# Kernel tuning notes

Measured on AMD Instinct MI355X. Metric: run time of the kernel, lower is better.

## Reference

```python
import jax, jax.numpy as jnp
import numpy as np

IN_DIM = 1024
HID = 256
OUT_DIM = 1000
NUM_BINS = 51
BATCH = 2048
N_LEGAL = 200


def setup_inputs() -> dict:
    key = jax.random.key(0)
    ks = jax.random.split(key, 12)
    s = lambda fan_in: 1.0 / np.sqrt(fan_in)
    u = lambda k, shp, b: jax.random.uniform(k, shp, jnp.float32, -b, b)
    return {
        "x": jax.random.normal(ks[0], (BATCH, IN_DIM), jnp.float32),
        # weights stored as [in, out] (math-equivalent to torch Linear)
        "w_in": u(ks[1], (IN_DIM, HID), s(IN_DIM)),
        "b_in": u(ks[2], (HID,), s(IN_DIM)),
        "w_ah": u(ks[3], (HID, HID), s(HID)),
        "b_ah": u(ks[4], (HID,), s(HID)),
        "w_ao": u(ks[5], (HID, OUT_DIM * NUM_BINS), s(HID)),
        "b_ao": u(ks[6], (OUT_DIM * NUM_BINS,), s(HID)),
        "w_vh": u(ks[7], (HID, HID), s(HID)),
        "b_vh": u(ks[8], (HID,), s(HID)),
        "w_vo": u(ks[9], (HID, NUM_BINS), s(HID)),
        "b_vo": u(ks[10], (NUM_BINS,), s(HID)),
        "v_range": jnp.linspace(-10.0, 10.0, NUM_BINS, dtype=jnp.float32),
        "possible_moves": jax.random.randint(ks[11], (BATCH, N_LEGAL), 0, OUT_DIM),
    }


def reference(x, w_in, b_in, w_ah, b_ah, w_ao, b_ao, w_vh, b_vh, w_vo, b_vo,
              v_range, possible_moves):
    B = x.shape[0]
    h = jax.nn.relu(x @ w_in + b_in)                       # [B, 256]
    adv_h = jax.nn.relu(h @ w_ah + b_ah)                   # [B, 256]
    val_h = jax.nn.relu(h @ w_vh + b_vh)                   # [B, 256]
    adv = (adv_h @ w_ao + b_ao).reshape(B, OUT_DIM, NUM_BINS)
    val = (val_h @ w_vo + b_vo).reshape(B, 1, NUM_BINS)
    q = val + adv - adv.mean(axis=1, keepdims=True)        # [B, A, bins]
    p = jnp.maximum(jax.nn.softmax(q, axis=2), 1e-5)       # softmax + clamp(min=1e-5)
    q_vals = jnp.sum(p * v_range, axis=2)                  # [B, A]
    # LegalSoftmax: per-row scatter of 1.0 at legal indices, vectorized
    mask = jnp.zeros((B, OUT_DIM), x.dtype).at[
        jnp.arange(B)[:, None], possible_moves].set(1.0)
    filtered = q_vals * mask
    # faithful to torch: any exact-zero entry (masked OR coincidental) -> -inf
    return jnp.where(filtered == 0, -jnp.inf, filtered)
```

## Files before the change

kernel.cpp:

```cpp
#include <hip/hip_runtime.h>
#include <cstdint>
#include <cstddef>

#define NB      2048
#define INDIM   1024
#define HID     256
#define NA      1000
#define BINS    51
#define NLEG    200
#define NPAIR   (NB*NLEG)
#define NBLK    256
#define PPB     (NPAIR/NBLK)

#define NEG_SENTINEL (-1.0e30f)

typedef float    f32x4  __attribute__((ext_vector_type(4)));
typedef __bf16   bf16x8 __attribute__((ext_vector_type(8)));
typedef unsigned short us8 __attribute__((ext_vector_type(8)));
typedef unsigned short us4 __attribute__((ext_vector_type(4)));
typedef unsigned long long u64x2 __attribute__((ext_vector_type(2)));

__device__ __forceinline__ unsigned short f2bf(float f) {
  union { float f; unsigned u; } v; v.f = f;
  return (unsigned short)((v.u + 0x7FFFu + ((v.u >> 16) & 1u)) >> 16);
}
__device__ __forceinline__ bf16x8 as_bf(us8 v) { return __builtin_bit_cast(bf16x8, v); }
__device__ __forceinline__ int imin(int a, int b) { return a < b ? a : b; }

__device__ __forceinline__ unsigned f2fp8x4(float a, float b, float c, float d) {
  int v = 0;
  v = __builtin_amdgcn_cvt_pk_fp8_f32(a, b, v, false);
  v = __builtin_amdgcn_cvt_pk_fp8_f32(c, d, v, true);
  return (unsigned)v;
}
__device__ __forceinline__ unsigned char f2fp8(float f) {
  int v = __builtin_amdgcn_cvt_pk_fp8_f32(f, 0.f, 0, false);
  return (unsigned char)(v & 0xff);
}
__device__ __forceinline__ float fp82f(unsigned char u) {
  return __builtin_amdgcn_cvt_f32_fp8((int)u, 0);
}

__global__ __launch_bounds__(256) void k_pre(
    const float* __restrict__ w_ao, unsigned char* __restrict__ wp8,
    float* __restrict__ wmean_acc,
    const float* __restrict__ w_in, const float* __restrict__ w_ah,
    const float* __restrict__ w_vh,
    unsigned short* __restrict__ w_inT, unsigned short* __restrict__ w_ahT,
    unsigned short* __restrict__ w_vhT,
    float* __restrict__ out, const int* __restrict__ pm,
    int* __restrict__ cnt,
    const float* __restrict__ x, unsigned short* __restrict__ x_bf) {
  __shared__ __align__(16) unsigned char smem[16320];
  int b = blockIdx.x, tid = threadIdx.x;
  if (b < 1000) {
    unsigned char* st = smem;
    int s = b & 7, a0 = (b >> 3) * 8;
    const float* wbase = w_ao + (size_t)(s * 32) * (NA * BINS) + a0 * BINS;
    for (int i = tid; i < 816; i += 256) {
      int kq = i / 102, c4 = i - kq * 102;
      const float* rp = wbase + (size_t)(kq * 4) * (NA * BINS) + c4 * 4;
      float4 f0 = *(const float4*)(rp);
      float4 f1 = *(const float4*)(rp + NA * BINS);
      float4 f2 = *(const float4*)(rp + 2 * NA * BINS);
      float4 f3 = *(const float4*)(rp + 3 * NA * BINS);
      unsigned pk0 = f2fp8x4(f0.x * 16.f, f0.y * 16.f, f0.z * 16.f, f0.w * 16.f);
      unsigned pk1 = f2fp8x4(f1.x * 16.f, f1.y * 16.f, f1.z * 16.f, f1.w * 16.f);
      unsigned pk2 = f2fp8x4(f2.x * 16.f, f2.y * 16.f, f2.z * 16.f, f2.w * 16.f);
      unsigned pk3 = f2fp8x4(f3.x * 16.f, f3.y * 16.f, f3.z * 16.f, f3.w * 16.f);
      unsigned s01lo = __builtin_amdgcn_perm(pk1, pk0, 0x05010400u);
      unsigned s01hi = __builtin_amdgcn_perm(pk1, pk0, 0x07030602u);
      unsigned s23lo = __builtin_amdgcn_perm(pk3, pk2, 0x05010400u);
      unsigned s23hi = __builtin_amdgcn_perm(pk3, pk2, 0x07030602u);
      unsigned o0 = __builtin_amdgcn_perm(s23lo, s01lo, 0x05040100u);
      unsigned o1 = __builtin_amdgcn_perm(s23lo, s01lo, 0x07060302u);
      unsigned o2 = __builtin_amdgcn_perm(s23hi, s01hi, 0x05040100u);
      unsigned o3 = __builtin_amdgcn_perm(s23hi, s01hi, 0x07060302u);
      int k4 = kq * 4;
      int swz = ((c4 >> 2) & 3) << 3;
      int kb = ((k4 & 24) ^ swz) + (k4 & 7);
      int cbase = c4 * 160;
      *(unsigned*)(st + cbase + kb)       = o0;
      *(unsigned*)(st + cbase + 40 + kb)  = o1;
      *(unsigned*)(st + cbase + 80 + kb)  = o2;
      *(unsigned*)(st + cbase + 120 + kb) = o3;
    }
    __syncthreads();
    for (int i = tid; i < 32 * 51; i += 256) {
      int r = i / 51, j = i - r * 51;
      float s8 = 0.f;
#pragma unroll
      for (int aL = 0; aL < 8; aL++) {
        int c = aL * 51 + j;
        s8 += fp82f(st[c * 40 + ((r & 24) ^ (((c >> 4) & 3) << 3)) + (r & 7)]);
      }
      atomicAdd(&wmean_acc[(size_t)(s * 32 + r) * BINS + j], s8);
    }
    int t4 = (tid >> 6) & 3, l = tid & 63;
    int col = t4 * 16 + (l & 15), kg = l >> 4;
    for (int aL = 0; aL < 8; aL++) {
      unsigned lo = 0, hi = 0;
      if (col < BINS) {
        int ci = aL * 51 + col;
        unsigned long long v8 = *(const unsigned long long*)(
            st + ci * 40 + ((kg * 8) ^ (((ci >> 4) & 3) << 3)));
        lo = (unsigned)v8; hi = (unsigned)(v8 >> 32);
      }
      uint2 v; v.x = lo; v.y = hi;
      *(uint2*)(wp8 + (size_t)(a0 + aL) * 16384 +
                (size_t)((s * 2 + (t4 >> 1)) * 64 + l) * 16 + (t4 & 1) * 8) = v;
    }
  } else if (b < 1384) {
    int bb = b - 1000;
    float (*tile)[33] = (float(*)[33])smem;
    const float* w; unsigned short* wT; int K, N, kt, nt;
    if (bb < 256)      { w = w_in; wT = w_inT; K = INDIM; N = HID; kt = bb & 31;        nt = bb >> 5; }
    else if (bb < 320) { w = w_ah; wT = w_ahT; K = HID;   N = HID; kt = (bb - 256) & 7; nt = (bb - 256) >> 3; }
    else               { w = w_vh; wT = w_vhT; K = HID;   N = HID; kt = (bb - 320) & 7; nt = (bb - 320) >> 3; }
    int k0 = kt * 32, n0 = nt * 32;
    int cr = tid >> 5, cc = tid & 31;
#pragma unroll
    for (int it = 0; it < 4; it++)
      tile[cr + it * 8][cc] = w[(size_t)(k0 + cr + it * 8) * N + n0 + cc];
    __syncthreads();
#pragma unroll
    for (int it = 0; it < 4; it++)
      wT[(size_t)(n0 + cr + it * 8) * K + k0 + cc] = f2bf(tile[cc][cr + it * 8]);
  } else if (b < 1884) {
    int base = (b - 1384) * 1024 + tid;
    float4 v = {NEG_SENTINEL, NEG_SENTINEL, NEG_SENTINEL, NEG_SENTINEL};
#pragma unroll
    for (int it = 0; it < 4; it++) ((float4*)out)[base + it * 256] = v;
  } else if (b < 2396) {
    int base4 = (b - 1884) * 1024 + tid;
#pragma unroll
    for (int it = 0; it < 4; it++) {
      float4 v = ((const float4*)x)[base4 + it * 256];
      us4 o;
      o[0] = f2bf(v.x); o[1] = f2bf(v.y); o[2] = f2bf(v.z); o[3] = f2bf(v.w);
      ((us4*)x_bf)[base4 + it * 256] = o;
    }
  } else {
    int* lh = (int*)smem;
    int blk = b - 2396;
    for (int i = tid; i < NA; i += 256) lh[i] = 0;
    __syncthreads();
    int base = blk * PPB;
    for (int i = tid; i < PPB; i += 256) atomicAdd(&lh[pm[base + i]], 1);
    __syncthreads();
    for (int a = tid; a < NA; a += 256) {
      int v = lh[a];
      if (v) atomicAdd(&cnt[a], v);
    }
  }
}

__global__ __launch_bounds__(256) void k_mid(
    const unsigned short* __restrict__ x_bf, const unsigned short* __restrict__ w_inT,
    const float* __restrict__ b_in, unsigned short* __restrict__ h_bf,
    const float* __restrict__ w_vo, const float* __restrict__ wmean_acc,
    const float* __restrict__ b_vo, const float* __restrict__ b_ao,
    unsigned short* __restrict__ Wc, float* __restrict__ bias_c,
    const int* __restrict__ cnt, int* __restrict__ off, int* __restrict__ cursor) {
  __shared__ __align__(16) char smem[1024];
  int b = blockIdx.x, tid = threadIdx.x;
  if (b < 512) {
    int w = tid >> 6, l = tid & 63, la = l & 15, g = l >> 4;
    int idx = b * 4 + w;
    int m0 = (idx & 127) * 16, n0 = (idx >> 7) * 16;
    f32x4 acc = {0.f, 0.f, 0.f, 0.f};
    const us8* Bp = (const us8*)(w_inT + (size_t)(n0 + la) * INDIM) + g;
    const us8* Ap = (const us8*)(x_bf + (size_t)(m0 + la) * INDIM) + g;
#pragma unroll 8
    for (int s = 0; s < 32; s++)
      acc = __builtin_amdgcn_mfma_f32_16x16x32_bf16(as_bf(Ap[s * 4]), as_bf(Bp[s * 4]),
                                                    acc, 0, 0, 0);
    float bb = b_in[n0 + la];
#pragma unroll
    for (int r = 0; r < 4; r++) {
      float v = fmaxf(acc[r] + bb, 0.f);
      h_bf[(size_t)(m0 + g * 4 + r) * HID + n0 + la] = f2bf(v);
    }
  } else if (b < 576) {
    float* sred = (float*)smem;
    int n = b - 512, t = tid;
    for (int k = t; k < 512; k += 256) {
      float v = 0.f;
      if (n < BINS)
        v = (k < 256) ? w_vo[(size_t)k * BINS + n]
                      : (-(0.001f / 16.f) * wmean_acc[(size_t)(k - 256) * BINS + n]);
      Wc[(size_t)n * 512 + k] = f2bf(v);
    }
    float acc = 0.f;
    if (n < BINS)
      for (int a = t; a < NA; a += 256) acc += b_ao[(size_t)a * BINS + n];
    sred[t] = acc;
    __syncthreads();
    for (int d = 128; d > 0; d >>= 1) { if (t < d) sred[t] += sred[t + d]; __syncthreads(); }
    if (t == 0) bias_c[n] = (n < BINS) ? (b_vo[n] - 0.001f * sred[0]) : 0.f;
  } else {
    int* s = (int*)smem;
    int t = tid, i0 = 4 * t;
    int v0 = (i0     < NA) ? cnt[i0]     : 0;
    int v1 = (i0 + 1 < NA) ? cnt[i0 + 1] : 0;
    int v2 = (i0 + 2 < NA) ? cnt[i0 + 2] : 0;
    int v3 = (i0 + 3 < NA) ? cnt[i0 + 3] : 0;
    int sum = v0 + v1 + v2 + v3;
    s[t] = sum;
    __syncthreads();
    for (int d = 1; d < 256; d <<= 1) {
      int u = (t >= d) ? s[t - d] : 0;
      __syncthreads();
      s[t] += u;
      __syncthreads();
    }
    int excl = s[t] - sum;
    if (i0     < NA) { off[i0]     = excl;                cursor[i0]     = excl; }
    if (i0 + 1 < NA) { off[i0 + 1] = excl + v0;           cursor[i0 + 1] = excl + v0; }
    if (i0 + 2 < NA) { off[i0 + 2] = excl + v0 + v1;      cursor[i0 + 2] = excl + v0 + v1; }
    if (i0 + 3 < NA) { off[i0 + 3] = excl + v0 + v1 + v2; cursor[i0 + 3] = excl + v0 + v1 + v2; }
  }
}

__global__ __launch_bounds__(256) void k_heads(
    const unsigned short* __restrict__ h,
    const unsigned short* __restrict__ wA, const float* __restrict__ bA,
    const unsigned short* __restrict__ wV, const float* __restrict__ bV,
    const unsigned short* __restrict__ Wc, const float* __restrict__ bias_c,
    unsigned char* __restrict__ Aext8, float* __restrict__ cbuf_f,
    const int* __restrict__ pm, int* __restrict__ cursor, int* __restrict__ rows) {
  __shared__ __align__(16) char smem[16896];
  int b = blockIdx.x, tid = threadIdx.x;
  if (b < 128) {
    unsigned short* aL = (unsigned short*)smem;
    unsigned short* vL = (unsigned short*)smem + 16 * 264;
    int w = tid >> 6, l = tid & 63, la = l & 15, g = l >> 4;
    int m0 = b * 16;
    const us8* Ap = (const us8*)(h + (size_t)(m0 + la) * HID) + g;
    us8 aF[8];
#pragma unroll
    for (int s = 0; s < 8; s++) aF[s] = Ap[s * 4];
#pragma unroll
    for (int part = 0; part < 2; part++) {
      const unsigned short* BT = part ? wV : wA;
      const float* bias = part ? bV : bA;
      unsigned short* oL = part ? vL : aL;
#pragma unroll
      for (int nt = 0; nt < 4; nt++) {
        int n0 = w * 64 + nt * 16;
        f32x4 acc = {0.f, 0.f, 0.f, 0.f};
        const us8* Bp = (const us8*)(BT + (size_t)(n0 + la) * HID) + g;
#pragma unroll
        for (int s = 0; s < 8; s++)
          acc = __builtin_amdgcn_mfma_f32_16x16x32_bf16(as_bf(aF[s]), as_bf(Bp[s * 4]),
                                                        acc, 0, 0, 0);
        float bb = bias[n0 + la];
#pragma unroll
        for (int r = 0; r < 4; r++) {
          float v = fmaxf(acc[r] + bb, 0.f);
          oL[(g * 4 + r) * 264 + n0 + la] = f2bf(v);
          if (part == 0)
            Aext8[(size_t)(m0 + g * 4 + r) * HID + n0 + la] = f2fp8(v);
        }
      }
    }
    __syncthreads();
    int n0c = w * 16;
    f32x4 acc = {0.f, 0.f, 0.f, 0.f};
    const us8* Vp  = (const us8*)(vL + la * 264) + g;
    const us8* Ap2 = (const us8*)(aL + la * 264) + g;
    const us8* BpV = (const us8*)(Wc + (size_t)(n0c + la) * 512) + g;
    const us8* BpA = (const us8*)(Wc + (size_t)(n0c + la) * 512 + 256) + g;
#pragma unroll
    for (int s = 0; s < 8; s++)
      acc = __builtin_amdgcn_mfma_f32_16x16x32_bf16(as_bf(Vp[s * 4]), as_bf(BpV[s * 4]),
                                                    acc, 0, 0, 0);
#pragma unroll
    for (int s = 0; s < 8; s++)
      acc = __builtin_amdgcn_mfma_f32_16x16x32_bf16(as_bf(Ap2[s * 4]), as_bf(BpA[s * 4]),
                                                    acc, 0, 0, 0);
    float bb = bias_c[n0c + la];
#pragma unroll
    for (int r = 0; r < 4; r++)
      cbuf_f[(size_t)(m0 + g * 4 + r) * 64 + n0c + la] = acc[r] + bb;
  } else {
    int* lc = (int*)smem;
    int* lbase = (int*)(smem + 4096);
    int blk = b - 128, t = tid;
    for (int i = t; i < NA; i += 256) lc[i] = 0;
    __syncthreads();
    int pbase = blk * PPB;
    for (int i = t; i < PPB; i += 256) atomicAdd(&lc[pm[pbase + i]], 1);
    __syncthreads();
    for (int i = t; i < NA; i += 256) {
      int v = lc[i];
      lbase[i] = v ? atomicAdd(&cursor[i], v) : 0;
      lc[i] = 0;
    }
    __syncthreads();
    for (int i = t; i < PPB; i += 256) {
      int a = pm[pbase + i];
      int r = atomicAdd(&lc[a], 1);
      rows[lbase[a] + r] = (pbase + i) / NLEG;
    }
  }
}

#define TILE_BODY(TILE, RA_) do {                                              \
  int rA = (RA_);                                                              \
  const long long* Ap = (const long long*)(Aext8 + (size_t)rA * HID) + g;      \
  const float4* cf = (const float4*)(cbuf_f + (size_t)rA * 64);                \
  long long a8[8];                                                             \
  _Pragma("unroll") for (int s = 0; s < 8; s++) a8[s] = Ap[s * 4];             \
  float4 cq0 = cf[g], cq1 = cf[4 + g], cq2 = cf[8 + g], cq3 = cf[12 + g];      \
  f32x4 acc0 = {0.f,0.f,0.f,0.f}, acc1 = {0.f,0.f,0.f,0.f};                    \
  f32x4 acc2 = {0.f,0.f,0.f,0.f}, acc3 = {0.f,0.f,0.f,0.f};                    \
  __builtin_amdgcn_s_setprio(1);                                               \
  _Pragma("unroll") for (int s = 0; s < 8; s++) {                              \
    u64x2 b01 = sBv[(s * 2) * 64 + l];                                         \
    u64x2 b23 = sBv[(s * 2 + 1) * 64 + l];                                     \
    acc0 = __builtin_amdgcn_mfma_f32_16x16x32_fp8_fp8(                         \
        (long long)b01[0], a8[s], acc0, 0, 0, 0);                              \
    acc1 = __builtin_amdgcn_mfma_f32_16x16x32_fp8_fp8(                         \
        (long long)b01[1], a8[s], acc1, 0, 0, 0);                              \
    acc2 = __builtin_amdgcn_mfma_f32_16x16x32_fp8_fp8(                         \
        (long long)b23[0], a8[s], acc2, 0, 0, 0);                              \
    acc3 = __builtin_amdgcn_mfma_f32_16x16x32_fp8_fp8(                         \
        (long long)b23[1], a8[s], acc3, 0, 0, 0);                              \
  }                                                                            \
  __builtin_amdgcn_s_setprio(0);                                               \
  float S = 0.f;                                                               \
  f32x4 e0, e1, e2, e3;                                                        \
  _Pragma("unroll") for (int r = 0; r < 4; r++) {                              \
    e0[r] = __expf(fmaf(acc0[r], 0.0625f, cq0[r] + bao0[r])); S += e0[r];      \
    e1[r] = __expf(fmaf(acc1[r], 0.0625f, cq1[r] + bao1[r])); S += e1[r];      \
    e2[r] = __expf(fmaf(acc2[r], 0.0625f, cq2[r] + bao2[r])); S += e2[r];      \
    e3[r] = __expf(fmaf(acc3[r], 0.0625f, cq3[r] + bao3[r])); S += e3[r];      \
  }                                                                            \
  S += __shfl_xor(S, 16); S += __shfl_xor(S, 32);                              \
  float inv = 1.f / S, qv = 0.f;                                               \
  _Pragma("unroll") for (int r = 0; r < 4; r++) {                              \
    int bin = g * 4 + r;                                                       \
    qv = fmaf(fmaxf(e0[r] * inv, 1e-5f), (float)bin * 0.4f - 10.f, qv);        \
    qv = fmaf(fmaxf(e1[r] * inv, 1e-5f), (float)(bin + 16) * 0.4f - 10.f, qv); \
    qv = fmaf(fmaxf(e2[r] * inv, 1e-5f), (float)(bin + 32) * 0.4f - 10.f, qv); \
    if (bin + 48 < BINS)                                                       \
      qv = fmaf(fmaxf(e3[r] * inv, 1e-5f), (float)(bin + 48) * 0.4f - 10.f, qv); \
  }                                                                            \
  qv += __shfl_xor(qv, 16); qv += __shfl_xor(qv, 32);                          \
  int gi = (TILE) * 16 + la;                                                   \
  if (g == 0 && gi < count)                                                    \
    out[(size_t)rA * NA + a] = (qv == 0.f) ? NEG_SENTINEL : qv;                \
} while (0)

__global__ __launch_bounds__(256) void k_main_mfma(
    const unsigned char* __restrict__ Aext8,
    const float* __restrict__ cbuf_f,
    const unsigned char* __restrict__ wp8,
    const float* __restrict__ b_ao,
    const int* __restrict__ cnt, const int* __restrict__ off,
    const int* __restrict__ rows,
    float* __restrict__ out) {
  __shared__ __align__(16) long long sB8[2048];
  const u64x2* sBv = (const u64x2*)sB8;
  int bx = blockIdx.x;
  int a = (bx & 7) * 125 + (bx >> 3);
  int count = cnt[a];
  int ntiles = (count + 15) >> 4;
  if ((int)(blockIdx.y * 4) >= ntiles) return;
  int tid = threadIdx.x;
  int w = tid >> 6, l = tid & 63, la = l & 15, g = l >> 4;
  int base = off[a];
  int t0 = blockIdx.y * 4 + w;

  int rQ0 = rows[base + imin( t0       * 16 + la, count - 1)];
  int rQ1 = rows[base + imin((t0 + 16) * 16 + la, count - 1)];

  const float* baop = b_ao + (size_t)a * BINS;
  f32x4 bao0, bao1, bao2, bao3;
#pragma unroll
  for (int r = 0; r < 4; r++) {
    int bin = g * 4 + r;
    bao0[r] = baop[bin];
    bao1[r] = baop[bin + 16];
    bao2[r] = baop[bin + 32];
    bao3[r] = (bin + 48 < BINS) ? baop[bin + 48] : NEG_SENTINEL;
  }

  const u64x2* wpa = (const u64x2*)(wp8 + (size_t)a * 16384);
#pragma unroll
  for (int i = 0; i < 4; i++) ((u64x2*)sB8)[tid + i * 256] = wpa[tid + i * 256];
  __syncthreads();

  if (t0      < ntiles) TILE_BODY(t0,      rQ0);
  if (t0 + 16 < ntiles) TILE_BODY(t0 + 16, rQ1);
  for (int tile = t0 + 32; tile < ntiles; tile += 16) {
    int rAt = rows[base + imin(tile * 16 + la, count - 1)];
    TILE_BODY(tile, rAt);
  }
}

extern "C" void kernel_launch(void* const* d_in, const int* in_sizes, int n_in,
                              void* d_out, int out_size, void* d_ws, size_t ws_size,
                              hipStream_t stream) {
  (void)in_sizes; (void)n_in; (void)out_size; (void)ws_size;
  const float* x     = (const float*)d_in[0];
  const float* w_in  = (const float*)d_in[1];
  const float* b_in  = (const float*)d_in[2];
  const float* w_ah  = (const float*)d_in[3];
  const float* b_ah  = (const float*)d_in[4];
  const float* w_ao  = (const float*)d_in[5];
  const float* b_ao  = (const float*)d_in[6];
  const float* w_vh  = (const float*)d_in[7];
  const float* b_vh  = (const float*)d_in[8];
  const float* w_vo  = (const float*)d_in[9];
  const float* b_vo  = (const float*)d_in[10];
  const int*   pm    = (const int*)d_in[12];
  float* out = (float*)d_out;

  char* p = (char*)d_ws;
  unsigned char*  wp8     = (unsigned char*)p;  p += (size_t)NA * 32 * 512;
  unsigned char*  Aext8   = (unsigned char*)p;  p += (size_t)NB * HID;
  unsigned short* h_bf    = (unsigned short*)p; p += (size_t)NB * HID * 2;
  unsigned short* w_inT   = (unsigned short*)p; p += (size_t)HID * INDIM * 2;
  unsigned short* w_ahT   = (unsigned short*)p; p += (size_t)HID * HID * 2;
  unsigned short* w_vhT   = (unsigned short*)p; p += (size_t)HID * HID * 2;
  unsigned short* Wc      = (unsigned short*)p; p += (size_t)64 * 512 * 2;
  unsigned short* x_bf    = (unsigned short*)p; p += (size_t)NB * INDIM * 2;
  float* bias_c = (float*)p; p += 64 * 4;
  float* cbuf_f = (float*)p; p += (size_t)NB * 64 * 4;
  float* wmean  = (float*)p; p += 13056 * 4;
  int* cnt    = (int*)p; p += NA * 4;
  int* off    = (int*)p; p += NA * 4;
  int* cursor = (int*)p; p += (size_t)NA * 4 + 240;
  int* rows   = (int*)p; p += (size_t)NPAIR * 4 + 256;

  hipMemsetAsync(wmean, 0, (13056 + NA) * sizeof(float), stream);

  k_pre<<<2652, 256, 0, stream>>>(w_ao, wp8, wmean, w_in, w_ah, w_vh,
                                  w_inT, w_ahT, w_vhT, out, pm, cnt, x, x_bf);
  k_mid<<<577, 256, 0, stream>>>(x_bf, w_inT, b_in, h_bf,
                                 w_vo, wmean, b_vo, b_ao, Wc, bias_c,
                                 cnt, off, cursor);
  k_heads<<<384, 256, 0, stream>>>(h_bf, w_ahT, b_ah, w_vhT, b_vh,
                                   Wc, bias_c, Aext8, cbuf_f,
                                   pm, cursor, rows);
  k_main_mfma<<<dim3(1000, 4), 256, 0, stream>>>(Aext8, cbuf_f, wp8, b_ao,
                                                 cnt, off, rows, out);
}
```

Baseline: 209.6 us.

## Collapse pipeline to three kernels with fixed-stride per-action row buckets

```diff
diff --git a/kernel.cpp b/kernel.cpp
--- a/kernel.cpp
+++ b/kernel.cpp
@@ -9,8 +9,8 @@
 #define BINS    51
 #define NLEG    200
 #define NPAIR   (NB*NLEG)
-#define NBLK    256
-#define PPB     (NPAIR/NBLK)
+#define PPB     (NPAIR/256)
+#define RSTRIDE 768
 
 #define NEG_SENTINEL (-1.0e30f)
 
@@ -37,25 +37,57 @@
   int v = __builtin_amdgcn_cvt_pk_fp8_f32(f, 0.f, 0, false);
   return (unsigned char)(v & 0xff);
 }
-__device__ __forceinline__ float fp82f(unsigned char u) {
-  return __builtin_amdgcn_cvt_f32_fp8((int)u, 0);
-}
 
 __global__ __launch_bounds__(256) void k_pre(
     const float* __restrict__ w_ao, unsigned char* __restrict__ wp8,
-    float* __restrict__ wmean_acc,
+    const float* __restrict__ w_vo, const float* __restrict__ b_vo,
+    const float* __restrict__ b_ao,
+    unsigned short* __restrict__ Wc, float* __restrict__ bias_c,
     const float* __restrict__ w_in, const float* __restrict__ w_ah,
     const float* __restrict__ w_vh,
     unsigned short* __restrict__ w_inT, unsigned short* __restrict__ w_ahT,
     unsigned short* __restrict__ w_vhT,
     float* __restrict__ out, const int* __restrict__ pm,
-    int* __restrict__ cnt,
+    int* __restrict__ cursor, int* __restrict__ rows,
     const float* __restrict__ x, unsigned short* __restrict__ x_bf) {
   __shared__ __align__(16) unsigned char smem[16320];
   int b = blockIdx.x, tid = threadIdx.x;
-  if (b < 1000) {
+  if (b < 256) {
+    float* red = (float*)smem;
+    int k = b;
+    const float* row = w_ao + (size_t)k * (NA * BINS);
+    float acc = 0.f;
+    if (tid < 255)
+      for (int i = tid; i < NA * BINS; i += 255) acc += row[i];
+    red[tid] = acc;
+    __syncthreads();
+    if (tid < 51) {
+      float S = red[tid] + red[tid + 51] + red[tid + 102] + red[tid + 153] +
+                red[tid + 204];
+      Wc[(size_t)tid * 512 + 256 + k] = f2bf(-0.001f * S);
+      Wc[(size_t)tid * 512 + k]       = f2bf(w_vo[(size_t)k * BINS + tid]);
+    } else if (tid < 64) {
+      Wc[(size_t)tid * 512 + 256 + k] = 0;
+      Wc[(size_t)tid * 512 + k]       = 0;
+    }
+  } else if (b == 256) {
+    float* red = (float*)smem;
+    float acc = 0.f;
+    if (tid < 255)
+      for (int i = tid; i < NA * BINS; i += 255) acc += b_ao[i];
+    red[tid] = acc;
+    __syncthreads();
+    if (tid < 51) {
+      float S = red[tid] + red[tid + 51] + red[tid + 102] + red[tid + 153] +
+                red[tid + 204];
+      bias_c[tid] = b_vo[tid] - 0.001f * S;
+    } else if (tid < 64) {
+      bias_c[tid] = 0.f;
+    }
+  } else if (b < 1257) {
     unsigned char* st = smem;
-    int s = b & 7, a0 = (b >> 3) * 8;
+    int bb = b - 257;
+    int s = bb & 7, a0 = (bb >> 3) * 8;
     const float* wbase = w_ao + (size_t)(s * 32) * (NA * BINS) + a0 * BINS;
     for (int i = tid; i < 816; i += 256) {
       int kq = i / 102, c4 = i - kq * 102;
@@ -86,16 +118,6 @@
       *(unsigned*)(st + cbase + 120 + kb) = o3;
     }
     __syncthreads();
-    for (int i = tid; i < 32 * 51; i += 256) {
-      int r = i / 51, j = i - r * 51;
-      float s8 = 0.f;
-#pragma unroll
-      for (int aL = 0; aL < 8; aL++) {
-        int c = aL * 51 + j;
-        s8 += fp82f(st[c * 40 + ((r & 24) ^ (((c >> 4) & 3) << 3)) + (r & 7)]);
-      }
-      atomicAdd(&wmean_acc[(size_t)(s * 32 + r) * BINS + j], s8);
-    }
     int t4 = (tid >> 6) & 3, l = tid & 63;
     int col = t4 * 16 + (l & 15), kg = l >> 4;
     for (int aL = 0; aL < 8; aL++) {
@@ -110,8 +132,28 @@
       *(uint2*)(wp8 + (size_t)(a0 + aL) * 16384 +
                 (size_t)((s * 2 + (t4 >> 1)) * 64 + l) * 16 + (t4 & 1) * 8) = v;
     }
-  } else if (b < 1384) {
-    int bb = b - 1000;
+  } else if (b < 1513) {
+    int* lc = (int*)smem;
+    int* lbase = (int*)(smem + 4096);
+    int blk = b - 1257, t = tid;
+    for (int i = t; i < NA; i += 256) lc[i] = 0;
+    __syncthreads();
+    int pbase = blk * PPB;
+    for (int i = t; i < PPB; i += 256) atomicAdd(&lc[pm[pbase + i]], 1);
+    __syncthreads();
+    for (int i = t; i < NA; i += 256) {
+      int v = lc[i];
+      lbase[i] = v ? atomicAdd(&cursor[i], v) : 0;
+      lc[i] = 0;
+    }
+    __syncthreads();
+    for (int i = t; i < PPB; i += 256) {
+      int a = pm[pbase + i];
+      int r = atomicAdd(&lc[a], 1);
+      rows[(size_t)a * RSTRIDE + lbase[a] + r] = (pbase + i) / NLEG;
+    }
+  } else if (b < 1897) {
+    int bb = b - 1513;
     float (*tile)[33] = (float(*)[33])smem;
     const float* w; unsigned short* wT; int K, N, kt, nt;
     if (bb < 256)      { w = w_in; wT = w_inT; K = INDIM; N = HID; kt = bb & 31;        nt = bb >> 5; }
@@ -126,13 +168,13 @@
 #pragma unroll
     for (int it = 0; it < 4; it++)
       wT[(size_t)(n0 + cr + it * 8) * K + k0 + cc] = f2bf(tile[cc][cr + it * 8]);
-  } else if (b < 1884) {
-    int base = (b - 1384) * 1024 + tid;
+  } else if (b < 2397) {
+    int base = (b - 1897) * 1024 + tid;
     float4 v = {NEG_SENTINEL, NEG_SENTINEL, NEG_SENTINEL, NEG_SENTINEL};
 #pragma unroll
     for (int it = 0; it < 4; it++) ((float4*)out)[base + it * 256] = v;
-  } else if (b < 2396) {
-    int base4 = (b - 1884) * 1024 + tid;
+  } else {
+    int base4 = (b - 2397) * 1024 + tid;
 #pragma unroll
     for (int it = 0; it < 4; it++) {
       float4 v = ((const float4*)x)[base4 + it * 256];
@@ -140,170 +182,100 @@
       o[0] = f2bf(v.x); o[1] = f2bf(v.y); o[2] = f2bf(v.z); o[3] = f2bf(v.w);
       ((us4*)x_bf)[base4 + it * 256] = o;
     }
-  } else {
-    int* lh = (int*)smem;
-    int blk = b - 2396;
-    for (int i = tid; i < NA; i += 256) lh[i] = 0;
-    __syncthreads();
-    int base = blk * PPB;
-    for (int i = tid; i < PPB; i += 256) atomicAdd(&lh[pm[base + i]], 1);
-    __syncthreads();
-    for (int a = tid; a < NA; a += 256) {
-      int v = lh[a];
-      if (v) atomicAdd(&cnt[a], v);
-    }
   }
 }
 
-__global__ __launch_bounds__(256) void k_mid(
+__global__ __launch_bounds__(256) void k_heads(
     const unsigned short* __restrict__ x_bf, const unsigned short* __restrict__ w_inT,
-    const float* __restrict__ b_in, unsigned short* __restrict__ h_bf,
-    const float* __restrict__ w_vo, const float* __restrict__ wmean_acc,
-    const float* __restrict__ b_vo, const float* __restrict__ b_ao,
-    unsigned short* __restrict__ Wc, float* __restrict__ bias_c,
-    const int* __restrict__ cnt, int* __restrict__ off, int* __restrict__ cursor) {
-  __shared__ __align__(16) char smem[1024];
-  int b = blockIdx.x, tid = threadIdx.x;
-  if (b < 512) {
-    int w = tid >> 6, l = tid & 63, la = l & 15, g = l >> 4;
-    int idx = b * 4 + w;
-    int m0 = (idx & 127) * 16, n0 = (idx >> 7) * 16;
-    f32x4 acc = {0.f, 0.f, 0.f, 0.f};
-    const us8* Bp = (const us8*)(w_inT + (size_t)(n0 + la) * INDIM) + g;
-    const us8* Ap = (const us8*)(x_bf + (size_t)(m0 + la) * INDIM) + g;
-#pragma unroll 8
-    for (int s = 0; s < 32; s++)
-      acc = __builtin_amdgcn_mfma_f32_16x16x32_bf16(as_bf(Ap[s * 4]), as_bf(Bp[s * 4]),
-                                                    acc, 0, 0, 0);
-    float bb = b_in[n0 + la];
-#pragma unroll
-    for (int r = 0; r < 4; r++) {
-      float v = fmaxf(acc[r] + bb, 0.f);
-      h_bf[(size_t)(m0 + g * 4 + r) * HID + n0 + la] = f2bf(v);
-    }
-  } else if (b < 576) {
-    float* sred = (float*)smem;
-    int n = b - 512, t = tid;
-    for (int k = t; k < 512; k += 256) {
-      float v = 0.f;
-      if (n < BINS)
-        v = (k < 256) ? w_vo[(size_t)k * BINS + n]
-                      : (-(0.001f / 16.f) * wmean_acc[(size_t)(k - 256) * BINS + n]);
-      Wc[(size_t)n * 512 + k] = f2bf(v);
-    }
-    float acc = 0.f;
-    if (n < BINS)
-      for (int a = t; a < NA; a += 256) acc += b_ao[(size_t)a * BINS + n];
-    sred[t] = acc;
-    __syncthreads();
-    for (int d = 128; d > 0; d >>= 1) { if (t < d) sred[t] += sred[t + d]; __syncthreads(); }
-    if (t == 0) bias_c[n] = (n < BINS) ? (b_vo[n] - 0.001f * sred[0]) : 0.f;
-  } else {
-    int* s = (int*)smem;
-    int t = tid, i0 = 4 * t;
-    int v0 = (i0     < NA) ? cnt[i0]     : 0;
-    int v1 = (i0 + 1 < NA) ? cnt[i0 + 1] : 0;
-    int v2 = (i0 + 2 < NA) ? cnt[i0 + 2] : 0;
-    int v3 = (i0 + 3 < NA) ? cnt[i0 + 3] : 0;
-    int sum = v0 + v1 + v2 + v3;
-    s[t] = sum;
-    __syncthreads();
-    for (int d = 1; d < 256; d <<= 1) {
-      int u = (t >= d) ? s[t - d] : 0;
-      __syncthreads();
-      s[t] += u;
-      __syncthreads();
-    }
-    int excl = s[t] - sum;
-    if (i0     < NA) { off[i0]     = excl;                cursor[i0]     = excl; }
-    if (i0 + 1 < NA) { off[i0 + 1] = excl + v0;           cursor[i0 + 1] = excl + v0; }
-    if (i0 + 2 < NA) { off[i0 + 2] = excl + v0 + v1;      cursor[i0 + 2] = excl + v0 + v1; }
-    if (i0 + 3 < NA) { off[i0 + 3] = excl + v0 + v1 + v2; cursor[i0 + 3] = excl + v0 + v1 + v2; }
-  }
-}
-
-__global__ __launch_bounds__(256) void k_heads(
-    const unsigned short* __restrict__ h,
+    const float* __restrict__ b_in,
     const unsigned short* __restrict__ wA, const float* __restrict__ bA,
     const unsigned short* __restrict__ wV, const float* __restrict__ bV,
     const unsigned short* __restrict__ Wc, const float* __restrict__ bias_c,
-    unsigned char* __restrict__ Aext8, float* __restrict__ cbuf_f,
-    const int* __restrict__ pm, int* __restrict__ cursor, int* __restrict__ rows) {
-  __shared__ __align__(16) char smem[16896];
+    unsigned char* __restrict__ Aext8, float* __restrict__ cbuf_f) {
+  __shared__ __align__(16) unsigned short hL[16 * 264];
+  __shared__ __align__(16) unsigned short aL[16 * 264];
+  __shared__ __align__(16) unsigned short vL[16 * 264];
   int b = blockIdx.x, tid = threadIdx.x;
-  if (b < 128) {
-    unsigned short* aL = (unsigned short*)smem;
-    unsigned short* vL = (unsigned short*)smem + 16 * 264;
-    int w = tid >> 6, l = tid & 63, la = l & 15, g = l >> 4;
-    int m0 = b * 16;
-    const us8* Ap = (const us8*)(h + (size_t)(m0 + la) * HID) + g;
-    us8 aF[8];
-#pragma unroll
-    for (int s = 0; s < 8; s++) aF[s] = Ap[s * 4];
-#pragma unroll
-    for (int part = 0; part < 2; part++) {
-      const unsigned short* BT = part ? wV : wA;
-      const float* bias = part ? bV : bA;
-      unsigned short* oL = part ? vL : aL;
-#pragma unroll
-      for (int nt = 0; nt < 4; nt++) {
-        int n0 = w * 64 + nt * 16;
-        f32x4 acc = {0.f, 0.f, 0.f, 0.f};
-        const us8* Bp = (const us8*)(BT + (size_t)(n0 + la) * HID) + g;
-#pragma unroll
-        for (int s = 0; s < 8; s++)
-          acc = __builtin_amdgcn_mfma_f32_16x16x32_bf16(as_bf(aF[s]), as_bf(Bp[s * 4]),
-                                                        acc, 0, 0, 0);
-        float bb = bias[n0 + la];
-#pragma unroll
-        for (int r = 0; r < 4; r++) {
-          float v = fmaxf(acc[r] + bb, 0.f);
-          oL[(g * 4 + r) * 264 + n0 + la] = f2bf(v);
-          if (part == 0)
-            Aext8[(size_t)(m0 + g * 4 + r) * HID + n0 + la] = f2fp8(v);
-        }
+  int w = tid >> 6, l = tid & 63, la = l & 15, g = l >> 4;
+  int m0 = b * 16;
+
+  {
+    const us8* Ax = (const us8*)(x_bf + (size_t)(m0 + la) * INDIM) + g;
+    const us8* B0 = (const us8*)(w_inT + (size_t)(w * 64 +  0 + la) * INDIM) + g;
+    const us8* B1 = (const us8*)(w_inT + (size_t)(w * 64 + 16 + la) * INDIM) + g;
+    const us8* B2 = (const us8*)(w_inT + (size_t)(w * 64 + 32 + la) * INDIM) + g;
+    const us8* B3 = (const us8*)(w_inT + (size_t)(w * 64 + 48 + la) * INDIM) + g;
+    f32x4 h0 = {0.f,0.f,0.f,0.f}, h1 = {0.f,0.f,0.f,0.f};
+    f32x4 h2 = {0.f,0.f,0.f,0.f}, h3 = {0.f,0.f,0.f,0.f};
+#pragma unroll 4
+    for (int s = 0; s < 32; s++) {
+      us8 xf = Ax[s * 4];
+      h0 = __builtin_amdgcn_mfma_f32_16x16x32_bf16(as_bf(xf), as_bf(B0[s * 4]), h0, 0, 0, 0);
+      h1 = __builtin_amdgcn_mfma_f32_16x16x32_bf16(as_bf(xf), as_bf(B1[s * 4]), h1, 0, 0, 0);
+      h2 = __builtin_amdgcn_mfma_f32_16x16x32_bf16(as_bf(xf), as_bf(B2[s * 4]), h2, 0, 0, 0);
+      h3 = __builtin_amdgcn_mfma_f32_16x16x32_bf16(as_bf(xf), as_bf(B3[s * 4]), h3, 0, 0, 0);
+    }
+    float bb0 = b_in[w * 64 +  0 + la], bb1 = b_in[w * 64 + 16 + la];
+    float bb2 = b_in[w * 64 + 32 + la], bb3 = b_in[w * 64 + 48 + la];
+#pragma unroll
+    for (int r = 0; r < 4; r++) {
+      int rw = (g * 4 + r) * 264 + w * 64 + la;
+      hL[rw]      = f2bf(fmaxf(h0[r] + bb0, 0.f));
+      hL[rw + 16] = f2bf(fmaxf(h1[r] + bb1, 0.f));
+      hL[rw + 32] = f2bf(fmaxf(h2[r] + bb2, 0.f));
+      hL[rw + 48] = f2bf(fmaxf(h3[r] + bb3, 0.f));
+    }
+  }
+  __syncthreads();
+
+  const us8* Ah = (const us8*)(hL + la * 264) + g;
+  us8 aF[8];
+#pragma unroll
+  for (int s = 0; s < 8; s++) aF[s] = Ah[s * 4];
+#pragma unroll
+  for (int part = 0; part < 2; part++) {
+    const unsigned short* BT = part ? wV : wA;
+    const float* bias = part ? bV : bA;
+    unsigned short* oL = part ? vL : aL;
+#pragma unroll
+    for (int nt = 0; nt < 4; nt++) {
+      int n0 = w * 64 + nt * 16;
+      f32x4 acc = {0.f, 0.f, 0.f, 0.f};
+      const us8* Bp = (const us8*)(BT + (size_t)(n0 + la) * HID) + g;
+#pragma unroll
+      for (int s = 0; s < 8; s++)
+        acc = __builtin_amdgcn_mfma_f32_16x16x32_bf16(as_bf(aF[s]), as_bf(Bp[s * 4]),
+                                                      acc, 0, 0, 0);
+      float bb = bias[n0 + la];
+#pragma unroll
+      for (int r = 0; r < 4; r++) {
+        float v = fmaxf(acc[r] + bb, 0.f);
+        oL[(g * 4 + r) * 264 + n0 + la] = f2bf(v);
+        if (part == 0)
+          Aext8[(size_t)(m0 + g * 4 + r) * HID + n0 + la] = f2fp8(v);
       }
     }
-    __syncthreads();
-    int n0c = w * 16;
-    f32x4 acc = {0.f, 0.f, 0.f, 0.f};
-    const us8* Vp  = (const us8*)(vL + la * 264) + g;
-    const us8* Ap2 = (const us8*)(aL + la * 264) + g;
-    const us8* BpV = (const us8*)(Wc + (size_t)(n0c + la) * 512) + g;
-    const us8* BpA = (const us8*)(Wc + (size_t)(n0c + la) * 512 + 256) + g;
-#pragma unroll
-    for (int s = 0; s < 8; s++)
-      acc = __builtin_amdgcn_mfma_f32_16x16x32_bf16(as_bf(Vp[s * 4]), as_bf(BpV[s * 4]),
-                                                    acc, 0, 0, 0);
-#pragma unroll
-    for (int s = 0; s < 8; s++)
-      acc = __builtin_amdgcn_mfma_f32_16x16x32_bf16(as_bf(Ap2[s * 4]), as_bf(BpA[s * 4]),
-                                                    acc, 0, 0, 0);
-    float bb = bias_c[n0c + la];
-#pragma unroll
-    for (int r = 0; r < 4; r++)
-      cbuf_f[(size_t)(m0 + g * 4 + r) * 64 + n0c + la] = acc[r] + bb;
-  } else {
-    int* lc = (int*)smem;
-    int* lbase = (int*)(smem + 4096);
-    int blk = b - 128, t = tid;
-    for (int i = t; i < NA; i += 256) lc[i] = 0;
-    __syncthreads();
-    int pbase = blk * PPB;
-    for (int i = t; i < PPB; i += 256) atomicAdd(&lc[pm[pbase + i]], 1);
-    __syncthreads();
-    for (int i = t; i < NA; i += 256) {
-      int v = lc[i];
-      lbase[i] = v ? atomicAdd(&cursor[i], v) : 0;
-      lc[i] = 0;
-    }
-    __syncthreads();
-    for (int i = t; i < PPB; i += 256) {
-      int a = pm[pbase + i];
-      int r = atomicAdd(&lc[a], 1);
-      rows[lbase[a] + r] = (pbase + i) / NLEG;
-    }
   }
+  __syncthreads();
+
+  int n0c = w * 16;
+  f32x4 acc = {0.f, 0.f, 0.f, 0.f};
+  const us8* Vp  = (const us8*)(vL + la * 264) + g;
+  const us8* Ap2 = (const us8*)(aL + la * 264) + g;
+  const us8* BpV = (const us8*)(Wc + (size_t)(n0c + la) * 512) + g;
+  const us8* BpA = (const us8*)(Wc + (size_t)(n0c + la) * 512 + 256) + g;
+#pragma unroll
+  for (int s = 0; s < 8; s++)
+    acc = __builtin_amdgcn_mfma_f32_16x16x32_bf16(as_bf(Vp[s * 4]), as_bf(BpV[s * 4]),
+                                                  acc, 0, 0, 0);
+#pragma unroll
+  for (int s = 0; s < 8; s++)
+    acc = __builtin_amdgcn_mfma_f32_16x16x32_bf16(as_bf(Ap2[s * 4]), as_bf(BpA[s * 4]),
+                                                  acc, 0, 0, 0);
+  float bb = bias_c[n0c + la];
+#pragma unroll
+  for (int r = 0; r < 4; r++)
+    cbuf_f[(size_t)(m0 + g * 4 + r) * 64 + n0c + la] = acc[r] + bb;
 }
 
 #define TILE_BODY(TILE, RA_) do {                                              \
@@ -358,7 +330,7 @@
     const float* __restrict__ cbuf_f,
     const unsigned char* __restrict__ wp8,
     const float* __restrict__ b_ao,
-    const int* __restrict__ cnt, const int* __restrict__ off,
+    const int* __restrict__ cnt,
     const int* __restrict__ rows,
     float* __restrict__ out) {
   __shared__ __align__(16) long long sB8[2048];
@@ -367,14 +339,16 @@
   int a = (bx & 7) * 125 + (bx >> 3);
   int count = cnt[a];
   int ntiles = (count + 15) >> 4;
-  if ((int)(blockIdx.y * 4) >= ntiles) return;
+  if (count == 0 || (int)(blockIdx.y * 4) >= ntiles) return;
   int tid = threadIdx.x;
   int w = tid >> 6, l = tid & 63, la = l & 15, g = l >> 4;
-  int base = off[a];
+  int base = a * RSTRIDE;
   int t0 = blockIdx.y * 4 + w;
 
   int rQ0 = rows[base + imin( t0       * 16 + la, count - 1)];
-  int rQ1 = rows[base + imin((t0 + 16) * 16 + la, count - 1)];
+  int rQ1 = rows[base + imin((t0 +  8) * 16 + la, count - 1)];
+  int rQ2 = rows[base + imin((t0 + 16) * 16 + la, count - 1)];
+  int rQ3 = rows[base + imin((t0 + 24) * 16 + la, count - 1)];
 
   const float* baop = b_ao + (size_t)a * BINS;
   f32x4 bao0, bao1, bao2, bao3;
@@ -393,8 +367,10 @@
   __syncthreads();
 
   if (t0      < ntiles) TILE_BODY(t0,      rQ0);
-  if (t0 + 16 < ntiles) TILE_BODY(t0 + 16, rQ1);
-  for (int tile = t0 + 32; tile < ntiles; tile += 16) {
+  if (t0 +  8 < ntiles) TILE_BODY(t0 +  8, rQ1);
+  if (t0 + 16 < ntiles) TILE_BODY(t0 + 16, rQ2);
+  if (t0 + 24 < ntiles) TILE_BODY(t0 + 24, rQ3);
+  for (int tile = t0 + 32; tile < ntiles; tile += 8) {
     int rAt = rows[base + imin(tile * 16 + la, count - 1)];
     TILE_BODY(tile, rAt);
   }
@@ -419,32 +395,25 @@
   float* out = (float*)d_out;
 
   char* p = (char*)d_ws;
-  unsigned char*  wp8     = (unsigned char*)p;  p += (size_t)NA * 32 * 512;
-  unsigned char*  Aext8   = (unsigned char*)p;  p += (size_t)NB * HID;
-  unsigned short* h_bf    = (unsigned short*)p; p += (size_t)NB * HID * 2;
-  unsigned short* w_inT   = (unsigned short*)p; p += (size_t)HID * INDIM * 2;
-  unsigned short* w_ahT   = (unsigned short*)p; p += (size_t)HID * HID * 2;
-  unsigned short* w_vhT   = (unsigned short*)p; p += (size_t)HID * HID * 2;
-  unsigned short* Wc      = (unsigned short*)p; p += (size_t)64 * 512 * 2;
-  unsigned short* x_bf    = (unsigned short*)p; p += (size_t)NB * INDIM * 2;
+  unsigned char*  wp8    = (unsigned char*)p;  p += (size_t)NA * 32 * 512;
+  unsigned char*  Aext8  = (unsigned char*)p;  p += (size_t)NB * HID;
+  unsigned short* w_inT  = (unsigned short*)p; p += (size_t)HID * INDIM * 2;
+  unsigned short* w_ahT  = (unsigned short*)p; p += (size_t)HID * HID * 2;
+  unsigned short* w_vhT  = (unsigned short*)p; p += (size_t)HID * HID * 2;
+  unsigned short* Wc     = (unsigned short*)p; p += (size_t)64 * 512 * 2;
+  unsigned short* x_bf   = (unsigned short*)p; p += (size_t)NB * INDIM * 2;
   float* bias_c = (float*)p; p += 64 * 4;
   float* cbuf_f = (float*)p; p += (size_t)NB * 64 * 4;
-  float* wmean  = (float*)p; p += 13056 * 4;
-  int* cnt    = (int*)p; p += NA * 4;
-  int* off    = (int*)p; p += NA * 4;
   int* cursor = (int*)p; p += (size_t)NA * 4 + 240;
-  int* rows   = (int*)p; p += (size_t)NPAIR * 4 + 256;
-
-  hipMemsetAsync(wmean, 0, (13056 + NA) * sizeof(float), stream);
-
-  k_pre<<<2652, 256, 0, stream>>>(w_ao, wp8, wmean, w_in, w_ah, w_vh,
-                                  w_inT, w_ahT, w_vhT, out, pm, cnt, x, x_bf);
-  k_mid<<<577, 256, 0, stream>>>(x_bf, w_inT, b_in, h_bf,
-                                 w_vo, wmean, b_vo, b_ao, Wc, bias_c,
-                                 cnt, off, cursor);
-  k_heads<<<384, 256, 0, stream>>>(h_bf, w_ahT, b_ah, w_vhT, b_vh,
-                                   Wc, bias_c, Aext8, cbuf_f,
-                                   pm, cursor, rows);
-  k_main_mfma<<<dim3(1000, 4), 256, 0, stream>>>(Aext8, cbuf_f, wp8, b_ao,
-                                                 cnt, off, rows, out);
-}
+  int* rows   = (int*)p; p += (size_t)NA * RSTRIDE * 4 + 256;
+
+  hipMemsetAsync(cursor, 0, NA * sizeof(int), stream);
+
+  k_pre<<<2909, 256, 0, stream>>>(w_ao, wp8, w_vo, b_vo, b_ao, Wc, bias_c,
+                                  w_in, w_ah, w_vh, w_inT, w_ahT, w_vhT,
+                                  out, pm, cursor, rows, x, x_bf);
+  k_heads<<<128, 256, 0, stream>>>(x_bf, w_inT, b_in, w_ahT, b_ah,
+                                   w_vhT, b_vh, Wc, bias_c, Aext8, cbuf_f);
+  k_main_mfma<<<dim3(1000, 2), 256, 0, stream>>>(Aext8, cbuf_f, wp8, b_ao,
+                                                 cursor, rows, out);
+}
```

New measurement: 267.0 us. +27.4%, slower.

## Replace histogram+prefix-scan bucketing with fixed-stride per-action row lists

Applied to the files above, without the earlier changes.

```diff
diff --git a/kernel.cpp b/kernel.cpp
--- a/kernel.cpp
+++ b/kernel.cpp
@@ -9,8 +9,8 @@
 #define BINS    51
 #define NLEG    200
 #define NPAIR   (NB*NLEG)
-#define NBLK    256
-#define PPB     (NPAIR/NBLK)
+#define PPB     (NPAIR/256)
+#define RSTRIDE 768
 
 #define NEG_SENTINEL (-1.0e30f)
 
@@ -48,8 +48,7 @@
     const float* __restrict__ w_vh,
     unsigned short* __restrict__ w_inT, unsigned short* __restrict__ w_ahT,
     unsigned short* __restrict__ w_vhT,
-    float* __restrict__ out, const int* __restrict__ pm,
-    int* __restrict__ cnt,
+    float* __restrict__ out,
     const float* __restrict__ x, unsigned short* __restrict__ x_bf) {
   __shared__ __align__(16) unsigned char smem[16320];
   int b = blockIdx.x, tid = threadIdx.x;
@@ -131,7 +130,7 @@
     float4 v = {NEG_SENTINEL, NEG_SENTINEL, NEG_SENTINEL, NEG_SENTINEL};
 #pragma unroll
     for (int it = 0; it < 4; it++) ((float4*)out)[base + it * 256] = v;
-  } else if (b < 2396) {
+  } else {
     int base4 = (b - 1884) * 1024 + tid;
 #pragma unroll
     for (int it = 0; it < 4; it++) {
@@ -140,18 +139,6 @@
       o[0] = f2bf(v.x); o[1] = f2bf(v.y); o[2] = f2bf(v.z); o[3] = f2bf(v.w);
       ((us4*)x_bf)[base4 + it * 256] = o;
     }
-  } else {
-    int* lh = (int*)smem;
-    int blk = b - 2396;
-    for (int i = tid; i < NA; i += 256) lh[i] = 0;
-    __syncthreads();
-    int base = blk * PPB;
-    for (int i = tid; i < PPB; i += 256) atomicAdd(&lh[pm[base + i]], 1);
-    __syncthreads();
-    for (int a = tid; a < NA; a += 256) {
-      int v = lh[a];
-      if (v) atomicAdd(&cnt[a], v);
-    }
   }
 }
 
@@ -160,8 +147,7 @@
     const float* __restrict__ b_in, unsigned short* __restrict__ h_bf,
     const float* __restrict__ w_vo, const float* __restrict__ wmean_acc,
     const float* __restrict__ b_vo, const float* __restrict__ b_ao,
-    unsigned short* __restrict__ Wc, float* __restrict__ bias_c,
-    const int* __restrict__ cnt, int* __restrict__ off, int* __restrict__ cursor) {
+    unsigned short* __restrict__ Wc, float* __restrict__ bias_c) {
   __shared__ __align__(16) char smem[1024];
   int b = blockIdx.x, tid = threadIdx.x;
   if (b < 512) {
@@ -181,7 +167,7 @@
       float v = fmaxf(acc[r] + bb, 0.f);
       h_bf[(size_t)(m0 + g * 4 + r) * HID + n0 + la] = f2bf(v);
     }
-  } else if (b < 576) {
+  } else {
     float* sred = (float*)smem;
     int n = b - 512, t = tid;
     for (int k = t; k < 512; k += 256) {
@@ -198,27 +184,6 @@
     __syncthreads();
     for (int d = 128; d > 0; d >>= 1) { if (t < d) sred[t] += sred[t + d]; __syncthreads(); }
     if (t == 0) bias_c[n] = (n < BINS) ? (b_vo[n] - 0.001f * sred[0]) : 0.f;
-  } else {
-    int* s = (int*)smem;
-    int t = tid, i0 = 4 * t;
-    int v0 = (i0     < NA) ? cnt[i0]     : 0;
-    int v1 = (i0 + 1 < NA) ? cnt[i0 + 1] : 0;
-    int v2 = (i0 + 2 < NA) ? cnt[i0 + 2] : 0;
-    int v3 = (i0 + 3 < NA) ? cnt[i0 + 3] : 0;
-    int sum = v0 + v1 + v2 + v3;
-    s[t] = sum;
-    __syncthreads();
-    for (int d = 1; d < 256; d <<= 1) {
-      int u = (t >= d) ? s[t - d] : 0;
-      __syncthreads();
-      s[t] += u;
-      __syncthreads();
-    }
-    int excl = s[t] - sum;
-    if (i0     < NA) { off[i0]     = excl;                cursor[i0]     = excl; }
-    if (i0 + 1 < NA) { off[i0 + 1] = excl + v0;           cursor[i0 + 1] = excl + v0; }
-    if (i0 + 2 < NA) { off[i0 + 2] = excl + v0 + v1;      cursor[i0 + 2] = excl + v0 + v1; }
-    if (i0 + 3 < NA) { off[i0 + 3] = excl + v0 + v1 + v2; cursor[i0 + 3] = excl + v0 + v1 + v2; }
   }
 }
 
@@ -301,7 +266,7 @@
     for (int i = t; i < PPB; i += 256) {
       int a = pm[pbase + i];
       int r = atomicAdd(&lc[a], 1);
-      rows[lbase[a] + r] = (pbase + i) / NLEG;
+      rows[(size_t)a * RSTRIDE + lbase[a] + r] = (pbase + i) / NLEG;
     }
   }
 }
@@ -358,7 +323,7 @@
     const float* __restrict__ cbuf_f,
     const unsigned char* __restrict__ wp8,
     const float* __restrict__ b_ao,
-    const int* __restrict__ cnt, const int* __restrict__ off,
+    const int* __restrict__ cnt,
     const int* __restrict__ rows,
     float* __restrict__ out) {
   __shared__ __align__(16) long long sB8[2048];
@@ -367,14 +332,16 @@
   int a = (bx & 7) * 125 + (bx >> 3);
   int count = cnt[a];
   int ntiles = (count + 15) >> 4;
-  if ((int)(blockIdx.y * 4) >= ntiles) return;
+  if (count == 0 || (int)(blockIdx.y * 4) >= ntiles) return;
   int tid = threadIdx.x;
   int w = tid >> 6, l = tid & 63, la = l & 15, g = l >> 4;
-  int base = off[a];
+  int base = a * RSTRIDE;
   int t0 = blockIdx.y * 4 + w;
 
   int rQ0 = rows[base + imin( t0       * 16 + la, count - 1)];
-  int rQ1 = rows[base + imin((t0 + 16) * 16 + la, count - 1)];
+  int rQ1 = rows[base + imin((t0 +  8) * 16 + la, count - 1)];
+  int rQ2 = rows[base + imin((t0 + 16) * 16 + la, count - 1)];
+  int rQ3 = rows[base + imin((t0 + 24) * 16 + la, count - 1)];
 
   const float* baop = b_ao + (size_t)a * BINS;
   f32x4 bao0, bao1, bao2, bao3;
@@ -393,8 +360,10 @@
   __syncthreads();
 
   if (t0      < ntiles) TILE_BODY(t0,      rQ0);
-  if (t0 + 16 < ntiles) TILE_BODY(t0 + 16, rQ1);
-  for (int tile = t0 + 32; tile < ntiles; tile += 16) {
+  if (t0 +  8 < ntiles) TILE_BODY(t0 +  8, rQ1);
+  if (t0 + 16 < ntiles) TILE_BODY(t0 + 16, rQ2);
+  if (t0 + 24 < ntiles) TILE_BODY(t0 + 24, rQ3);
+  for (int tile = t0 + 32; tile < ntiles; tile += 8) {
     int rAt = rows[base + imin(tile * 16 + la, count - 1)];
     TILE_BODY(tile, rAt);
   }
@@ -419,32 +388,29 @@
   float* out = (float*)d_out;
 
   char* p = (char*)d_ws;
-  unsigned char*  wp8     = (unsigned char*)p;  p += (size_t)NA * 32 * 512;
-  unsigned char*  Aext8   = (unsigned char*)p;  p += (size_t)NB * HID;
-  unsigned short* h_bf    = (unsigned short*)p; p += (size_t)NB * HID * 2;
-  unsigned short* w_inT   = (unsigned short*)p; p += (size_t)HID * INDIM * 2;
-  unsigned short* w_ahT   = (unsigned short*)p; p += (size_t)HID * HID * 2;
-  unsigned short* w_vhT   = (unsigned short*)p; p += (size_t)HID * HID * 2;
-  unsigned short* Wc      = (unsigned short*)p; p += (size_t)64 * 512 * 2;
-  unsigned short* x_bf    = (unsigned short*)p; p += (size_t)NB * INDIM * 2;
+  unsigned char*  wp8    = (unsigned char*)p;  p += (size_t)NA * 32 * 512;
+  unsigned char*  Aext8  = (unsigned char*)p;  p += (size_t)NB * HID;
+  unsigned short* h_bf   = (unsigned short*)p; p += (size_t)NB * HID * 2;
+  unsigned short* w_inT  = (unsigned short*)p; p += (size_t)HID * INDIM * 2;
+  unsigned short* w_ahT  = (unsigned short*)p; p += (size_t)HID * HID * 2;
+  unsigned short* w_vhT  = (unsigned short*)p; p += (size_t)HID * HID * 2;
+  unsigned short* Wc     = (unsigned short*)p; p += (size_t)64 * 512 * 2;
+  unsigned short* x_bf   = (unsigned short*)p; p += (size_t)NB * INDIM * 2;
   float* bias_c = (float*)p; p += 64 * 4;
   float* cbuf_f = (float*)p; p += (size_t)NB * 64 * 4;
   float* wmean  = (float*)p; p += 13056 * 4;
-  int* cnt    = (int*)p; p += NA * 4;
-  int* off    = (int*)p; p += NA * 4;
   int* cursor = (int*)p; p += (size_t)NA * 4 + 240;
-  int* rows   = (int*)p; p += (size_t)NPAIR * 4 + 256;
+  int* rows   = (int*)p; p += (size_t)NA * RSTRIDE * 4 + 256;
 
   hipMemsetAsync(wmean, 0, (13056 + NA) * sizeof(float), stream);
 
-  k_pre<<<2652, 256, 0, stream>>>(w_ao, wp8, wmean, w_in, w_ah, w_vh,
-                                  w_inT, w_ahT, w_vhT, out, pm, cnt, x, x_bf);
-  k_mid<<<577, 256, 0, stream>>>(x_bf, w_inT, b_in, h_bf,
-                                 w_vo, wmean, b_vo, b_ao, Wc, bias_c,
-                                 cnt, off, cursor);
+  k_pre<<<2396, 256, 0, stream>>>(w_ao, wp8, wmean, w_in, w_ah, w_vh,
+                                  w_inT, w_ahT, w_vhT, out, x, x_bf);
+  k_mid<<<576, 256, 0, stream>>>(x_bf, w_inT, b_in, h_bf,
+                                 w_vo, wmean, b_vo, b_ao, Wc, bias_c);
   k_heads<<<384, 256, 0, stream>>>(h_bf, w_ahT, b_ah, w_vhT, b_vh,
                                    Wc, bias_c, Aext8, cbuf_f,
                                    pm, cursor, rows);
-  k_main_mfma<<<dim3(1000, 4), 256, 0, stream>>>(Aext8, cbuf_f, wp8, b_ao,
-                                                 cnt, off, rows, out);
-}
+  k_main_mfma<<<dim3(1000, 2), 256, 0, stream>>>(Aext8, cbuf_f, wp8, b_ao,
+                                                 cursor, rows, out);
+}
```

After: 201.1 us, median of 2. 4.1% less time.
